# Kernel optimization log

Measured on AMD Instinct MI355X. Metric: run time of the kernel, lower is better.

## Reference

```python
import jax, jax.numpy as jnp
import numpy as np

H, K, D = 24, 2, 128          # query heads, kv heads, head_size
HIDDEN = H * D                # 3072
ROPE_THETA = 10000.0


def setup_inputs() -> dict:
    key = jax.random.key(0)
    ks = jax.random.split(key, 6)
    B, S = 2, 2048
    T = B * S
    hidden_states = jax.random.normal(ks[0], (T, HIDDEN), dtype=jnp.float32)
    w_qkv = jax.random.normal(ks[1], ((H + 2 * K) * D, HIDDEN), dtype=jnp.float32) * (HIDDEN ** -0.5)
    b_qkv = jax.random.normal(ks[2], ((H + 2 * K) * D,), dtype=jnp.float32) * 0.02
    w_o = jax.random.normal(ks[3], (HIDDEN, H * D), dtype=jnp.float32) * (HIDDEN ** -0.5)
    b_o = jax.random.normal(ks[4], (HIDDEN,), dtype=jnp.float32) * 0.02
    # rotary tables: positions restart per sequence (flash-varlen prefill layout)
    pos = jnp.tile(jnp.arange(S, dtype=jnp.float32), B)            # [T]
    inv_freq = 1.0 / (ROPE_THETA ** (jnp.arange(0, D, 2, dtype=jnp.float32) / D))  # [D/2]
    freqs = pos[:, None] * inv_freq[None, :]                        # [T, D/2]
    return {
        "hidden_states": hidden_states,
        "w_qkv": w_qkv, "b_qkv": b_qkv,
        "w_o": w_o, "b_o": b_o,
        "cos": jnp.cos(freqs), "sin": jnp.sin(freqs),
        "seq_len": S, "window": 1024,
    }


def _rope(x, cos, sin):
    # rotate-half (neox) style, as in TGI PositionRotaryEmbedding
    half = x.shape[-1] // 2
    x1, x2 = x[..., :half], x[..., half:]
    c, s = cos[:, None, :], sin[:, None, :]   # broadcast over head dim
    return jnp.concatenate([x1 * c - x2 * s, x2 * c + x1 * s], axis=-1)


def reference(hidden_states, w_qkv, b_qkv, w_o, b_o, cos, sin, seq_len, window):
    T = hidden_states.shape[0]
    B = T // seq_len
    scale = D ** -0.5

    # fused QKV projection
    qkv = hidden_states @ w_qkv.T + b_qkv                 # [T, (H+2K)*D]
    q = qkv[:, : H * D].reshape(T, H, D)
    kv = qkv[:, H * D:].reshape(T, 2, K, D)
    k, v = kv[:, 0], kv[:, 1]                             # [T, K, D]

    q = _rope(q, cos, sin)
    k = _rope(k, cos, sin)

    # GQA: expand kv heads to query heads
    groups = H // K
    qb = q.reshape(B, seq_len, H, D)
    kb = jnp.repeat(k.reshape(B, seq_len, K, D), groups, axis=2)  # [B,S,H,D]
    vb = jnp.repeat(v.reshape(B, seq_len, K, D), groups, axis=2)

    scores = jnp.einsum("bqhd,bkhd->bhqk", qb, kb) * scale        # [B,H,S,S]
    idx = jnp.arange(seq_len)
    delta = idx[:, None] - idx[None, :]
    mask = (delta >= 0) & (delta < window)                        # causal + sliding window
    scores = jnp.where(mask[None, None], scores, jnp.float32(-1e9))
    attn = jax.nn.softmax(scores, axis=-1)
    out = jnp.einsum("bhqk,bkhd->bqhd", attn, vb).reshape(T, H * D)
    return out @ w_o.T + b_o
```

## Files before the change

### kernel.cpp

```cpp
#include <hip/hip_runtime.h>
#include <hip/hip_bf16.h>

typedef __attribute__((ext_vector_type(8))) short bf16x8;
typedef __attribute__((ext_vector_type(4))) float f32x4;

__device__ __forceinline__ short f2bf_bits(float f) {
    __hip_bfloat16 h = __float2bfloat16(f);
    short s;
    __builtin_memcpy(&s, &h, 2);
    return s;
}

__device__ __forceinline__ float bf_bits2f(short s) {
    unsigned int u = ((unsigned int)(unsigned short)s) << 16;
    float f;
    __builtin_memcpy(&f, &u, 4);
    return f;
}

__device__ __forceinline__ bf16x8 load8(const float* p) {
    float4 a = *(const float4*)p;
    float4 b = *(const float4*)(p + 4);
    bf16x8 r;
    r[0] = f2bf_bits(a.x); r[1] = f2bf_bits(a.y);
    r[2] = f2bf_bits(a.z); r[3] = f2bf_bits(a.w);
    r[4] = f2bf_bits(b.x); r[5] = f2bf_bits(b.y);
    r[6] = f2bf_bits(b.z); r[7] = f2bf_bits(b.w);
    return r;
}
__device__ __forceinline__ bf16x8 load8(const __hip_bfloat16* p) {
    return *(const bf16x8*)p;
}

__device__ __forceinline__ void store_out(__hip_bfloat16* p, float v) {
    *p = __float2bfloat16(v);
}
__device__ __forceinline__ void store_out(float* p, float v) { *p = v; }

__global__ void cvt3_f32_bf16(const float* __restrict__ a, short* __restrict__ da, int na8,
                              const float* __restrict__ b, short* __restrict__ db, int nb8,
                              const float* __restrict__ c, short* __restrict__ dc, int nc8) {
    int i = blockIdx.x * 256 + threadIdx.x;
    if (i < na8) {
        *(bf16x8*)(da + (size_t)i * 8) = load8(a + (size_t)i * 8);
    } else if ((i -= na8) < nb8) {
        *(bf16x8*)(db + (size_t)i * 8) = load8(b + (size_t)i * 8);
    } else if ((i -= nb8) < nc8) {
        *(bf16x8*)(dc + (size_t)i * 8) = load8(c + (size_t)i * 8);
    }
}

#define GB_REG 65536

__device__ __forceinline__ int half_off(int buf, int half) {
    return buf * 32768 + half * 16384;
}

template <typename TC>
__global__ __launch_bounds__(512) void gemm256(
    const __hip_bfloat16* __restrict__ A, const __hip_bfloat16* __restrict__ B,
    const float* __restrict__ bias, TC* __restrict__ C, int M, int N, int K)
{
    __shared__ char smem[131072];

    const int tid  = threadIdx.x;
    const int lane = tid & 63;
    const int wid  = tid >> 6;
    const int quad = lane >> 4;
    const int m16  = lane & 15;
    const int wmg  = wid >> 2;
    const int wng  = wid & 3;
    const int bhalf = wng >> 1;
    const int bsub  = (wng & 1) * 4;

    const int gx  = gridDim.x;
    const int nwg = gx * gridDim.y;
    int lin = blockIdx.y * gx + blockIdx.x;
    if ((nwg & 7) == 0) {
        int q = nwg >> 3;
        lin = (lin & 7) * q + (lin >> 3);
    }
    const int bn = lin % gx, bm = lin / gx;
    const int mBase = bm * 256, nBase = bn * 256;

    const int roff = (m16 << 6) | ((quad * 16) ^ ((m16 & 8) << 2));

    int r_s[2], c_s[2];
    #pragma unroll
    for (int l = 0; l < 2; ++l) {
        int sub = l * 8 + wid;
        int r16 = (tid >> 2) & 15;
        int cb  = ((tid & 3) * 16) ^ ((r16 & 8) << 2);
        r_s[l] = (sub >> 1) * 16 + r16;
        c_s[l] = (sub & 1) * 32 + (cb >> 1);
    }

    const __hip_bfloat16* Ab = A + (size_t)mBase * K;
    const __hip_bfloat16* Bb = B + (size_t)nBase * K;

    auto stage = [&](int region, const __hip_bfloat16* base, int buf, int half, int tile) {
        const __hip_bfloat16* gb = base + (size_t)(half * 128) * K + tile * 64;
        #pragma unroll
        for (int l = 0; l < 2; ++l) {
            const __hip_bfloat16* g = gb + (size_t)r_s[l] * K + c_s[l];
            short* lb = (short*)(smem + region + half_off(buf, half) + l * 8192 + wid * 1024);
            __builtin_amdgcn_global_load_lds(
                (__attribute__((address_space(1))) void*)g,
                (__attribute__((address_space(3))) void*)lb, 16, 0, 0);
        }
    };

    f32x4 acc[8][4] = {};
    bf16x8 afr[4][2];
    bf16x8 bfr[2][2][2];

    auto LD_A = [&](int buf, int g) {
        const char* base = smem + half_off(buf, wmg) + (g ? 8192 : 0);
        #pragma unroll
        for (int m = 0; m < 4; ++m)
            #pragma unroll
            for (int ks = 0; ks < 2; ++ks)
                afr[m][ks] = *(const bf16x8*)(base + ((m * 2 + ks) << 10) + roff);
    };
    auto LD_B = [&](int buf, int g) {
        const char* base = smem + GB_REG + half_off(buf, bhalf) + ((bsub + g * 2) << 11);
        #pragma unroll
        for (int j = 0; j < 2; ++j)
            #pragma unroll
            for (int ks = 0; ks < 2; ++ks)
                bfr[g][j][ks] = *(const bf16x8*)(base + ((j * 2 + ks) << 10) + roff);
    };
    auto MM = [&](int mo, int g) {
        #pragma unroll
        for (int m = 0; m < 4; ++m)
            #pragma unroll
            for (int j = 0; j < 2; ++j)
                #pragma unroll
                for (int ks = 0; ks < 2; ++ks)
                    acc[mo + m][g * 2 + j] = __builtin_amdgcn_mfma_f32_16x16x32_bf16(
                        afr[m][ks], bfr[g][j][ks], acc[mo + m][g * 2 + j], 0, 0, 0);
    };

#define SBAR() __builtin_amdgcn_s_barrier()
#define WAIT_LGKM0() do { asm volatile("s_waitcnt lgkmcnt(0)" ::: "memory"); \
                          __builtin_amdgcn_sched_barrier(0); } while (0)
#define WAIT_VM4()   do { asm volatile("s_waitcnt vmcnt(4)"   ::: "memory"); \
                          __builtin_amdgcn_sched_barrier(0); } while (0)

    const int NT = K >> 6;

    stage(GB_REG, Bb, 0, 0, 0);
    stage(0,      Ab, 0, 0, 0);
    stage(GB_REG, Bb, 0, 1, 0);
    stage(0,      Ab, 0, 1, 0);
    stage(GB_REG, Bb, 1, 0, 1);
    stage(0,      Ab, 1, 0, 1);
    WAIT_VM4();
    SBAR();

    for (int i = 0; i < (NT >> 1); ++i) {
        const int to = 2 * i + 1;
        const int t2 = min(2 * i + 2, NT - 1);
        const int t3 = min(2 * i + 3, NT - 1);
        LD_A(0, 0); LD_B(0, 0);
        stage(GB_REG, Bb, 1, 1, to);
        SBAR(); WAIT_LGKM0();
        __builtin_amdgcn_s_setprio(1); MM(0, 0); __builtin_amdgcn_s_setprio(0);
        SBAR();
        LD_B(0, 1);
        stage(0, Ab, 1, 1, to);
        SBAR(); WAIT_LGKM0();
        __builtin_amdgcn_s_setprio(1); MM(0, 1); __builtin_amdgcn_s_setprio(0);
        SBAR();
        LD_A(0, 1);
        stage(GB_REG, Bb, 0, 0, t2);
        SBAR(); WAIT_LGKM0();
        __builtin_amdgcn_s_setprio(1); MM(4, 1); __builtin_amdgcn_s_setprio(0);
        SBAR();
        stage(0, Ab, 0, 0, t2);
        WAIT_VM4();
        SBAR();
        __builtin_amdgcn_s_setprio(1); MM(4, 0); __builtin_amdgcn_s_setprio(0);
        SBAR();
        LD_A(1, 0); LD_B(1, 0);
        stage(GB_REG, Bb, 0, 1, t2);
        SBAR(); WAIT_LGKM0();
        __builtin_amdgcn_s_setprio(1); MM(0, 0); __builtin_amdgcn_s_setprio(0);
        SBAR();
        LD_B(1, 1);
        stage(0, Ab, 0, 1, t2);
        SBAR(); WAIT_LGKM0();
        __builtin_amdgcn_s_setprio(1); MM(0, 1); __builtin_amdgcn_s_setprio(0);
        SBAR();
        LD_A(1, 1);
        stage(GB_REG, Bb, 1, 0, t3);
        SBAR(); WAIT_LGKM0();
        __builtin_amdgcn_s_setprio(1); MM(4, 1); __builtin_amdgcn_s_setprio(0);
        SBAR();
        stage(0, Ab, 1, 0, t3);
        WAIT_VM4();
        SBAR();
        __builtin_amdgcn_s_setprio(1); MM(4, 0); __builtin_amdgcn_s_setprio(0);
        SBAR();
    }

#undef SBAR
#undef WAIT_LGKM0
#undef WAIT_VM4

    float bv[4];
    #pragma unroll
    for (int j = 0; j < 4; ++j)
        bv[j] = bias[nBase + wng * 64 + j * 16 + m16];

    #pragma unroll
    for (int mf = 0; mf < 8; ++mf) {
        #pragma unroll
        for (int j = 0; j < 4; ++j) {
            const int col = nBase + wng * 64 + j * 16 + m16;
            #pragma unroll
            for (int r = 0; r < 4; ++r) {
                const int row = mBase + wmg * 128 + mf * 16 + quad * 4 + r;
                store_out(&C[(size_t)row * N + col], acc[mf][j][r] + bv[j]);
            }
        }
    }
}

#define LDSS 40

template <typename TA, typename TB, typename TC>
__global__ __launch_bounds__(256) void gemm_bt_bias(
    const TA* __restrict__ A, const TB* __restrict__ B,
    const float* __restrict__ bias, TC* __restrict__ C, int M, int N, int K)
{
    __shared__ short As[128 * LDSS];
    __shared__ short Bs[128 * LDSS];

    const int tid  = threadIdx.x;
    const int lane = tid & 63;
    const int wid  = tid >> 6;
    const int quad = lane >> 4;
    const int m16  = lane & 15;

    const int mBase = blockIdx.y * 128;
    const int nBase = blockIdx.x * 128;
    const int wm = (wid >> 1) * 64;
    const int wn = (wid & 1) * 64;

    f32x4 acc[4][4] = {};
    const int srow = tid >> 2;
    const int sgrp = (tid & 3) * 8;

    for (int kt = 0; kt < K; kt += 32) {
        __syncthreads();
        for (int p = 0; p < 2; ++p) {
            int r = srow + p * 64;
            *(bf16x8*)(&As[r * LDSS + sgrp]) =
                load8(A + (size_t)(mBase + r) * K + kt + sgrp);
            *(bf16x8*)(&Bs[r * LDSS + sgrp]) =
                load8(B + (size_t)(nBase + r) * K + kt + sgrp);
        }
        __syncthreads();

        bf16x8 afr[4], bfr[4];
        #pragma unroll
        for (int i = 0; i < 4; ++i)
            afr[i] = *(const bf16x8*)(&As[(wm + 16 * i + m16) * LDSS + quad * 8]);
        #pragma unroll
        for (int j = 0; j < 4; ++j)
            bfr[j] = *(const bf16x8*)(&Bs[(wn + 16 * j + m16) * LDSS + quad * 8]);
        #pragma unroll
        for (int i = 0; i < 4; ++i)
            #pragma unroll
            for (int j = 0; j < 4; ++j)
                acc[i][j] = __builtin_amdgcn_mfma_f32_16x16x32_bf16(
                    afr[i], bfr[j], acc[i][j], 0, 0, 0);
    }

    float bv[4];
    #pragma unroll
    for (int j = 0; j < 4; ++j)
        bv[j] = bias[nBase + wn + 16 * j + m16];

    #pragma unroll
    for (int i = 0; i < 4; ++i)
        #pragma unroll
        for (int j = 0; j < 4; ++j) {
            int col = nBase + wn + 16 * j + m16;
            #pragma unroll
            for (int r = 0; r < 4; ++r) {
                int row = mBase + wm + 16 * i + quad * 4 + r;
                store_out(&C[(size_t)row * N + col], acc[i][j][r] + bv[j]);
            }
        }
}

__global__ void rope_kernel(__hip_bfloat16* __restrict__ qkv,
                            const float* __restrict__ cosb,
                            const float* __restrict__ sinb, int T)
{
    int idx = blockIdx.x * 256 + threadIdx.x;
    int total = T * 26 * 8;
    if (idx >= total) return;
    int j = idx & 7;
    int h = (idx >> 3) % 26;
    int t = idx / (26 * 8);
    int col = (h < 24) ? h * 128 : 3072 + (h - 24) * 128;
    int d0 = j * 8;
    size_t base = (size_t)t * 3584 + col + d0;
    bf16x8 x1 = *(const bf16x8*)((const short*)qkv + base);
    bf16x8 x2 = *(const bf16x8*)((const short*)qkv + base + 64);
    float4 c0 = *(const float4*)(cosb + t * 64 + d0);
    float4 c1 = *(const float4*)(cosb + t * 64 + d0 + 4);
    float4 s0 = *(const float4*)(sinb + t * 64 + d0);
    float4 s1 = *(const float4*)(sinb + t * 64 + d0 + 4);
    float cc[8] = {c0.x, c0.y, c0.z, c0.w, c1.x, c1.y, c1.z, c1.w};
    float ss[8] = {s0.x, s0.y, s0.z, s0.w, s1.x, s1.y, s1.z, s1.w};
    bf16x8 o1, o2;
    #pragma unroll
    for (int i = 0; i < 8; ++i) {
        float f1 = bf_bits2f(x1[i]);
        float f2 = bf_bits2f(x2[i]);
        o1[i] = f2bf_bits(f1 * cc[i] - f2 * ss[i]);
        o2[i] = f2bf_bits(f2 * cc[i] + f1 * ss[i]);
    }
    *(bf16x8*)((short*)qkv + base)      = o1;
    *(bf16x8*)((short*)qkv + base + 64) = o2;
}

#define SM_SHIFT 12.0f

__global__ __launch_bounds__(256, 3) void attn_kernel(
    const __hip_bfloat16* __restrict__ qkv,
    __hip_bfloat16* __restrict__ out,
    const int* __restrict__ seq_len_p, const int* __restrict__ window_p)
{
    const int S = seq_len_p[0];
    const int window = window_p[0];
    const float scale = 0.088388347648318447f;

    const int h   = blockIdx.y;
    const int kvh = h / 12;
    const int tid  = threadIdx.x;
    const int lane = tid & 63;
    const int wid  = tid >> 6;
    const int quad = lane >> 4;
    const int m16  = lane & 15;

    const int qb_global = blockIdx.x * 128;
    const int b  = qb_global / S;
    const int qb = qb_global - b * S;

    __shared__ short Vt[128 * 72];
    __shared__ short Ps[4][32 * 40];

    const size_t kvrow0 = (size_t)(b * S) * 3584 + 3072 + kvh * 128;

    bf16x8 qf[2][4];
    {
        const __hip_bfloat16* qp =
            qkv + (size_t)(qb_global + wid * 32 + m16) * 3584 + h * 128;
        #pragma unroll
        for (int qt = 0; qt < 2; ++qt)
            #pragma unroll
            for (int dc = 0; dc < 4; ++dc)
                qf[qt][dc] = *(const bf16x8*)(qp + qt * 16 * 3584 + dc * 32 + quad * 8);
    }

    f32x4 accO[2][8] = {};
    float lqt[2] = {0.f, 0.f};

    int ka0 = qb - window + 1;
    if (ka0 < 0) ka0 = 0;
    ka0 &= ~31;
    const int kend = qb + 128;

    for (int kt = ka0; kt < kend; kt += 32) {
        __syncthreads();
        #pragma unroll
        for (int p = 0; p < 2; ++p) {
            int L   = tid + p * 256;
            int key = L & 31;
            int gg  = L >> 5;
            int d0  = gg * 8;
            bf16x8 v8 = *(const bf16x8*)(qkv + kvrow0 + (size_t)(kt + key) * 3584 + 256 + d0);
            short* dst = &Vt[d0 * 72 + key + (gg & 1) * 32];
            #pragma unroll
            for (int i2 = 0; i2 < 8; ++i2) dst[i2 * 72] = v8[i2];
        }
        __syncthreads();

        f32x4 sacc[2][2] = {};
        #pragma unroll
        for (int st = 0; st < 2; ++st) {
            const __hip_bfloat16* kp =
                qkv + kvrow0 + (size_t)(kt + st * 16 + m16) * 3584;
            #pragma unroll
            for (int dc = 0; dc < 4; ++dc) {
                bf16x8 kf = *(const bf16x8*)(kp + dc * 32 + quad * 8);
                sacc[st][0] = __builtin_amdgcn_mfma_f32_16x16x32_bf16(
                    kf, qf[0][dc], sacc[st][0], 0, 0, 0);
                sacc[st][1] = __builtin_amdgcn_mfma_f32_16x16x32_bf16(
                    kf, qf[1][dc], sacc[st][1], 0, 0, 0);
            }
        }

        #pragma unroll
        for (int qt = 0; qt < 2; ++qt) {
            const int qmin = qb + wid * 32 + qt * 16;
            short* prow = &Ps[wid][(qt * 16 + m16) * 40];
            float psum = 0.f;
            if (kt <= qmin - 31 && kt >= qmin + 16 - window) {
                #pragma unroll
                for (int st = 0; st < 2; ++st)
                    #pragma unroll
                    for (int r = 0; r < 4; ++r) {
                        float pp = __expf(fminf(
                            sacc[st][qt][r] * scale - SM_SHIFT, 80.f));
                        psum += pp;
                        prow[st * 16 + quad * 4 + r] = f2bf_bits(pp);
                    }
            } else {
                const int dl_base = (qmin + m16) - (kt + quad * 4);
                #pragma unroll
                for (int st = 0; st < 2; ++st)
                    #pragma unroll
                    for (int r = 0; r < 4; ++r) {
                        int dl = dl_base - st * 16 - r;
                        float pp = ((unsigned)dl < (unsigned)window)
                            ? __expf(fminf(sacc[st][qt][r] * scale - SM_SHIFT, 80.f))
                            : 0.f;
                        psum += pp;
                        prow[st * 16 + quad * 4 + r] = f2bf_bits(pp);
                    }
            }
            psum += __shfl_xor(psum, 16, 64);
            psum += __shfl_xor(psum, 32, 64);
            lqt[qt] += psum;
        }

        bf16x8 pf0 = *(const bf16x8*)(&Ps[wid][(0  + m16) * 40 + quad * 8]);
        bf16x8 pf1 = *(const bf16x8*)(&Ps[wid][(16 + m16) * 40 + quad * 8]);
        #pragma unroll
        for (int dt = 0; dt < 8; ++dt) {
            int row = dt * 16 + m16;
            bf16x8 vf = *(const bf16x8*)(&Vt[row * 72 + quad * 8 + ((row >> 3) & 1) * 32]);
            accO[0][dt] = __builtin_amdgcn_mfma_f32_16x16x32_bf16(pf0, vf, accO[0][dt], 0, 0, 0);
            accO[1][dt] = __builtin_amdgcn_mfma_f32_16x16x32_bf16(pf1, vf, accO[1][dt], 0, 0, 0);
        }
    }

    #pragma unroll
    for (int qt = 0; qt < 2; ++qt) {
        float li[4];
        #pragma unroll
        for (int r = 0; r < 4; ++r)
            li[r] = 1.0f / __shfl(lqt[qt], quad * 4 + r, 64);
        #pragma unroll
        for (int r = 0; r < 4; ++r) {
            int t = qb_global + wid * 32 + qt * 16 + quad * 4 + r;
            __hip_bfloat16* op = out + (size_t)t * 3072 + h * 128 + m16;
            #pragma unroll
            for (int dt = 0; dt < 8; ++dt)
                op[dt * 16] = __float2bfloat16(accO[qt][dt][r] * li[r]);
        }
    }
}

extern "C" void kernel_launch(void* const* d_in, const int* in_sizes, int n_in,
                              void* d_out, int out_size, void* d_ws, size_t ws_size,
                              hipStream_t stream) {
    const float* hidden = (const float*)d_in[0];
    const float* w_qkv  = (const float*)d_in[1];
    const float* b_qkv  = (const float*)d_in[2];
    const float* w_o    = (const float*)d_in[3];
    const float* b_o    = (const float*)d_in[4];
    const float* cosb   = (const float*)d_in[5];
    const float* sinb   = (const float*)d_in[6];
    const int* seq_len_p = (const int*)d_in[7];
    const int* window_p  = (const int*)d_in[8];

    const int HID  = in_sizes[4];
    const int NQKV = in_sizes[2];
    const int T    = in_sizes[0] / HID;

    size_t off = 0;
    auto alloc = [&](size_t bytes) {
        char* p = (char*)d_ws + off;
        off = (off + bytes + 255) & ~(size_t)255;
        return p;
    };
    __hip_bfloat16* qkv      = (__hip_bfloat16*)alloc((size_t)T * NQKV * 2);
    __hip_bfloat16* attn_out = (__hip_bfloat16*)alloc((size_t)T * HID * 2);
    __hip_bfloat16* hid_bf = (__hip_bfloat16*)alloc((size_t)T * HID * 2);
    __hip_bfloat16* wq_bf  = (__hip_bfloat16*)alloc((size_t)NQKV * HID * 2);
    __hip_bfloat16* wo_bf  = (__hip_bfloat16*)alloc((size_t)HID * HID * 2);
    const bool pre = (ws_size >= off);
    const bool big = pre && (T % 256 == 0) && (NQKV % 256 == 0) &&
                     (HID % 256 == 0) && (HID % 64 == 0);

    dim3 blk(256);

    if (big) {
        int n8h = T * HID / 8, n8q = NQKV * HID / 8, n8o = HID * HID / 8;
        int n8 = n8h + n8q + n8o;
        cvt3_f32_bf16<<<dim3((n8 + 255) / 256), blk, 0, stream>>>(
            hidden, (short*)hid_bf, n8h, w_qkv, (short*)wq_bf, n8q,
            w_o, (short*)wo_bf, n8o);
        gemm256<__hip_bfloat16><<<dim3(NQKV / 256, T / 256), dim3(512), 0, stream>>>(
            hid_bf, wq_bf, b_qkv, qkv, T, NQKV, HID);
    } else {
        gemm_bt_bias<float, float, __hip_bfloat16>
            <<<dim3(NQKV / 128, T / 128), blk, 0, stream>>>(
            hidden, w_qkv, b_qkv, qkv, T, NQKV, HID);
    }

    int total = T * 26 * 8;
    rope_kernel<<<dim3((total + 255) / 256), blk, 0, stream>>>(qkv, cosb, sinb, T);

    attn_kernel<<<dim3(T / 128, 24), blk, 0, stream>>>(qkv, attn_out, seq_len_p, window_p);

    if (big) {
        gemm256<float><<<dim3(HID / 256, T / 256), dim3(512), 0, stream>>>(
            attn_out, wo_bf, b_o, (float*)d_out, T, HID, HID);
    } else {
        gemm_bt_bias<__hip_bfloat16, float, float>
            <<<dim3(HID / 128, T / 128), blk, 0, stream>>>(
            attn_out, w_o, b_o, (float*)d_out, T, HID, HID);
    }
}
```

Before: 479.5 us.

## Double-buffer V tiles and prefetch K into registers in attention loop

The attention kernel now prefetches the next K tile into registers and the next V tile into a second LDS buffer while computing on the current one, leaving a single barrier per iteration. Query blocks are launched in reverse order so the blocks with the longest key ranges start first, and MFMA sections are wrapped in s_setprio. The intent is to hide global-load latency behind the MFMA work. In exchange, register and LDS use rise, so launch bounds drop from 3 to 2 blocks per CU, which lowers occupancy.

After: 484.1 us. No clear change (+1.0%).

```diff
diff --git a/kernel.cpp b/kernel.cpp
--- a/kernel.cpp
+++ b/kernel.cpp
@@ -331,7 +331,7 @@
 
 #define SM_SHIFT 12.0f
 
-__global__ __launch_bounds__(256, 3) void attn_kernel(
+__global__ __launch_bounds__(256, 2) void attn_kernel(
     const __hip_bfloat16* __restrict__ qkv,
     __hip_bfloat16* __restrict__ out,
     const int* __restrict__ seq_len_p, const int* __restrict__ window_p)
@@ -348,11 +348,13 @@
     const int quad = lane >> 4;
     const int m16  = lane & 15;
 
-    const int qb_global = blockIdx.x * 128;
-    const int b  = qb_global / S;
-    const int qb = qb_global - b * S;
-
-    __shared__ short Vt[128 * 72];
+    const int nbb = S >> 7;
+    const int b   = blockIdx.x / nbb;
+    const int ib  = blockIdx.x - b * nbb;
+    const int qb  = (nbb - 1 - ib) << 7;
+    const int qb_global = b * S + qb;
+
+    __shared__ short Vt[2][128 * 72];
     __shared__ short Ps[4][32 * 40];
 
     const size_t kvrow0 = (size_t)(b * S) * 3584 + 3072 + kvh * 128;
@@ -375,35 +377,67 @@
     if (ka0 < 0) ka0 = 0;
     ka0 &= ~31;
     const int kend = qb + 128;
-
-    for (int kt = ka0; kt < kend; kt += 32) {
-        __syncthreads();
-        #pragma unroll
-        for (int p = 0; p < 2; ++p) {
-            int L   = tid + p * 256;
-            int key = L & 31;
-            int gg  = L >> 5;
-            int d0  = gg * 8;
-            bf16x8 v8 = *(const bf16x8*)(qkv + kvrow0 + (size_t)(kt + key) * 3584 + 256 + d0);
-            short* dst = &Vt[d0 * 72 + key + (gg & 1) * 32];
-            #pragma unroll
-            for (int i2 = 0; i2 < 8; ++i2) dst[i2 * 72] = v8[i2];
-        }
-        __syncthreads();
+    const int niter = (kend - ka0) >> 5;
+
+    const int skey = tid & 31;
+    const int sgg0 = tid >> 5;
+    const int sgg1 = sgg0 + 8;
+
+    bf16x8 vnx0, vnx1;
+    vnx0 = *(const bf16x8*)(qkv + kvrow0 + (size_t)(ka0 + skey) * 3584 + 256 + sgg0 * 8);
+    vnx1 = *(const bf16x8*)(qkv + kvrow0 + (size_t)(ka0 + skey) * 3584 + 256 + sgg1 * 8);
+    bf16x8 kreg[2][4];
+    {
+        const __hip_bfloat16* kp = qkv + kvrow0 + (size_t)ka0 * 3584;
+        #pragma unroll
+        for (int st = 0; st < 2; ++st)
+            #pragma unroll
+            for (int dc = 0; dc < 4; ++dc)
+                kreg[st][dc] = *(const bf16x8*)(kp + (size_t)(st * 16 + m16) * 3584 + dc * 32 + quad * 8);
+    }
+    {
+        short* dst0 = &Vt[0][(sgg0 * 8) * 72 + skey + (sgg0 & 1) * 32];
+        short* dst1 = &Vt[0][(sgg1 * 8) * 72 + skey + (sgg1 & 1) * 32];
+        #pragma unroll
+        for (int i2 = 0; i2 < 8; ++i2) dst0[i2 * 72] = vnx0[i2];
+        #pragma unroll
+        for (int i2 = 0; i2 < 8; ++i2) dst1[i2 * 72] = vnx1[i2];
+    }
+    asm volatile("s_waitcnt lgkmcnt(0)" ::: "memory");
+    __builtin_amdgcn_s_barrier();
+    __builtin_amdgcn_sched_barrier(0);
+
+    for (int it = 0; it < niter; ++it) {
+        const int kt  = ka0 + it * 32;
+        const int buf = it & 1;
+        const bool notlast = (it + 1 < niter);
+        const int ktn = notlast ? kt + 32 : kt;
+
+        if (notlast) {
+            vnx0 = *(const bf16x8*)(qkv + kvrow0 + (size_t)(ktn + skey) * 3584 + 256 + sgg0 * 8);
+            vnx1 = *(const bf16x8*)(qkv + kvrow0 + (size_t)(ktn + skey) * 3584 + 256 + sgg1 * 8);
+        }
 
         f32x4 sacc[2][2] = {};
-        #pragma unroll
-        for (int st = 0; st < 2; ++st) {
-            const __hip_bfloat16* kp =
-                qkv + kvrow0 + (size_t)(kt + st * 16 + m16) * 3584;
+        __builtin_amdgcn_s_setprio(1);
+        #pragma unroll
+        for (int st = 0; st < 2; ++st)
             #pragma unroll
             for (int dc = 0; dc < 4; ++dc) {
-                bf16x8 kf = *(const bf16x8*)(kp + dc * 32 + quad * 8);
                 sacc[st][0] = __builtin_amdgcn_mfma_f32_16x16x32_bf16(
-                    kf, qf[0][dc], sacc[st][0], 0, 0, 0);
+                    kreg[st][dc], qf[0][dc], sacc[st][0], 0, 0, 0);
                 sacc[st][1] = __builtin_amdgcn_mfma_f32_16x16x32_bf16(
-                    kf, qf[1][dc], sacc[st][1], 0, 0, 0);
+                    kreg[st][dc], qf[1][dc], sacc[st][1], 0, 0, 0);
             }
+        __builtin_amdgcn_s_setprio(0);
+
+        if (notlast) {
+            const __hip_bfloat16* kp = qkv + kvrow0 + (size_t)ktn * 3584;
+            #pragma unroll
+            for (int st = 0; st < 2; ++st)
+                #pragma unroll
+                for (int dc = 0; dc < 4; ++dc)
+                    kreg[st][dc] = *(const bf16x8*)(kp + (size_t)(st * 16 + m16) * 3584 + dc * 32 + quad * 8);
         }
 
         #pragma unroll
@@ -440,15 +474,32 @@
             lqt[qt] += psum;
         }
 
-        bf16x8 pf0 = *(const bf16x8*)(&Ps[wid][(0  + m16) * 40 + quad * 8]);
-        bf16x8 pf1 = *(const bf16x8*)(&Ps[wid][(16 + m16) * 40 + quad * 8]);
-        #pragma unroll
-        for (int dt = 0; dt < 8; ++dt) {
-            int row = dt * 16 + m16;
-            bf16x8 vf = *(const bf16x8*)(&Vt[row * 72 + quad * 8 + ((row >> 3) & 1) * 32]);
-            accO[0][dt] = __builtin_amdgcn_mfma_f32_16x16x32_bf16(pf0, vf, accO[0][dt], 0, 0, 0);
-            accO[1][dt] = __builtin_amdgcn_mfma_f32_16x16x32_bf16(pf1, vf, accO[1][dt], 0, 0, 0);
-        }
+        {
+            bf16x8 pf0 = *(const bf16x8*)(&Ps[wid][(0  + m16) * 40 + quad * 8]);
+            bf16x8 pf1 = *(const bf16x8*)(&Ps[wid][(16 + m16) * 40 + quad * 8]);
+            __builtin_amdgcn_s_setprio(1);
+            #pragma unroll
+            for (int dt = 0; dt < 8; ++dt) {
+                int row = dt * 16 + m16;
+                bf16x8 vf = *(const bf16x8*)(&Vt[buf][row * 72 + quad * 8 + ((row >> 3) & 1) * 32]);
+                accO[0][dt] = __builtin_amdgcn_mfma_f32_16x16x32_bf16(pf0, vf, accO[0][dt], 0, 0, 0);
+                accO[1][dt] = __builtin_amdgcn_mfma_f32_16x16x32_bf16(pf1, vf, accO[1][dt], 0, 0, 0);
+            }
+            __builtin_amdgcn_s_setprio(0);
+        }
+
+        if (notlast) {
+            short* dst0 = &Vt[buf ^ 1][(sgg0 * 8) * 72 + skey + (sgg0 & 1) * 32];
+            short* dst1 = &Vt[buf ^ 1][(sgg1 * 8) * 72 + skey + (sgg1 & 1) * 32];
+            #pragma unroll
+            for (int i2 = 0; i2 < 8; ++i2) dst0[i2 * 72] = vnx0[i2];
+            #pragma unroll
+            for (int i2 = 0; i2 < 8; ++i2) dst1[i2 * 72] = vnx1[i2];
+        }
+
+        asm volatile("s_waitcnt lgkmcnt(0)" ::: "memory");
+        __builtin_amdgcn_s_barrier();
+        __builtin_amdgcn_sched_barrier(0);
     }
 
     #pragma unroll
```

## Halve attention query tile to 64, reverse block order, prefetch V before barrier

Applied to the files above, without the earlier changes.

The attention kernel now processes 64 query rows per block (16 per wave) instead of 128, doubling the grid and raising the occupancy target to 4 blocks per CU. Blocks are issued in reverse order within each sequence, so the longer causal tiles start first. V loads are issued before the barrier using raw s_barrier with an explicit waitcnt, and the PV MFMAs are wrapped in setprio to favour the matrix work. Smaller tiles give more parallelism and less register pressure, but each K/V tile is reused by fewer queries, which raises K/V load traffic per output row.

Result: slower. 644.0 us (+34.3%).

```diff
diff --git a/kernel.cpp b/kernel.cpp
--- a/kernel.cpp
+++ b/kernel.cpp
@@ -331,7 +331,7 @@
 
 #define SM_SHIFT 12.0f
 
-__global__ __launch_bounds__(256, 3) void attn_kernel(
+__global__ __launch_bounds__(256, 4) void attn_kernel(
     const __hip_bfloat16* __restrict__ qkv,
     __hip_bfloat16* __restrict__ out,
     const int* __restrict__ seq_len_p, const int* __restrict__ window_p)
@@ -348,50 +348,60 @@
     const int quad = lane >> 4;
     const int m16  = lane & 15;
 
-    const int qb_global = blockIdx.x * 128;
-    const int b  = qb_global / S;
-    const int qb = qb_global - b * S;
+    const int nbb = S >> 6;
+    const int b   = blockIdx.x / nbb;
+    const int ib  = blockIdx.x - b * nbb;
+    const int qb  = (nbb - 1 - ib) << 6;
+    const int qb_global = b * S + qb;
 
     __shared__ short Vt[128 * 72];
-    __shared__ short Ps[4][32 * 40];
+    __shared__ short Ps[4][16 * 40];
 
     const size_t kvrow0 = (size_t)(b * S) * 3584 + 3072 + kvh * 128;
 
-    bf16x8 qf[2][4];
+    bf16x8 qf[4];
     {
         const __hip_bfloat16* qp =
-            qkv + (size_t)(qb_global + wid * 32 + m16) * 3584 + h * 128;
-        #pragma unroll
-        for (int qt = 0; qt < 2; ++qt)
-            #pragma unroll
-            for (int dc = 0; dc < 4; ++dc)
-                qf[qt][dc] = *(const bf16x8*)(qp + qt * 16 * 3584 + dc * 32 + quad * 8);
-    }
-
-    f32x4 accO[2][8] = {};
-    float lqt[2] = {0.f, 0.f};
+            qkv + (size_t)(qb_global + wid * 16 + m16) * 3584 + h * 128;
+        #pragma unroll
+        for (int dc = 0; dc < 4; ++dc)
+            qf[dc] = *(const bf16x8*)(qp + dc * 32 + quad * 8);
+    }
+
+    f32x4 accO[8] = {};
+    float lq = 0.f;
 
     int ka0 = qb - window + 1;
     if (ka0 < 0) ka0 = 0;
     ka0 &= ~31;
-    const int kend = qb + 128;
-
-    for (int kt = ka0; kt < kend; kt += 32) {
-        __syncthreads();
-        #pragma unroll
-        for (int p = 0; p < 2; ++p) {
-            int L   = tid + p * 256;
-            int key = L & 31;
-            int gg  = L >> 5;
-            int d0  = gg * 8;
-            bf16x8 v8 = *(const bf16x8*)(qkv + kvrow0 + (size_t)(kt + key) * 3584 + 256 + d0);
-            short* dst = &Vt[d0 * 72 + key + (gg & 1) * 32];
-            #pragma unroll
-            for (int i2 = 0; i2 < 8; ++i2) dst[i2 * 72] = v8[i2];
-        }
-        __syncthreads();
-
-        f32x4 sacc[2][2] = {};
+    const int kend = qb + 64;
+    const int niter = (kend - ka0) >> 5;
+
+    const int skey = tid & 31;
+    const int sgg0 = tid >> 5;
+    const int sgg1 = sgg0 + 8;
+
+    for (int it = 0; it < niter; ++it) {
+        const int kt = ka0 + it * 32;
+
+        bf16x8 v0 = *(const bf16x8*)(qkv + kvrow0 + (size_t)(kt + skey) * 3584 + 256 + sgg0 * 8);
+        bf16x8 v1 = *(const bf16x8*)(qkv + kvrow0 + (size_t)(kt + skey) * 3584 + 256 + sgg1 * 8);
+
+        __builtin_amdgcn_s_barrier();
+
+        {
+            short* dst0 = &Vt[(sgg0 * 8) * 72 + skey + (sgg0 & 1) * 32];
+            short* dst1 = &Vt[(sgg1 * 8) * 72 + skey + (sgg1 & 1) * 32];
+            #pragma unroll
+            for (int i2 = 0; i2 < 8; ++i2) dst0[i2 * 72] = v0[i2];
+            #pragma unroll
+            for (int i2 = 0; i2 < 8; ++i2) dst1[i2 * 72] = v1[i2];
+        }
+        asm volatile("s_waitcnt lgkmcnt(0)" ::: "memory");
+        __builtin_amdgcn_s_barrier();
+        __builtin_amdgcn_sched_barrier(0);
+
+        f32x4 sacc[2] = {};
         #pragma unroll
         for (int st = 0; st < 2; ++st) {
             const __hip_bfloat16* kp =
@@ -399,17 +409,14 @@
             #pragma unroll
             for (int dc = 0; dc < 4; ++dc) {
                 bf16x8 kf = *(const bf16x8*)(kp + dc * 32 + quad * 8);
-                sacc[st][0] = __builtin_amdgcn_mfma_f32_16x16x32_bf16(
-                    kf, qf[0][dc], sacc[st][0], 0, 0, 0);
-                sacc[st][1] = __builtin_amdgcn_mfma_f32_16x16x32_bf16(
-                    kf, qf[1][dc], sacc[st][1], 0, 0, 0);
+                sacc[st] = __builtin_amdgcn_mfma_f32_16x16x32_bf16(
+                    kf, qf[dc], sacc[st], 0, 0, 0);
             }
         }
 
-        #pragma unroll
-        for (int qt = 0; qt < 2; ++qt) {
-            const int qmin = qb + wid * 32 + qt * 16;
-            short* prow = &Ps[wid][(qt * 16 + m16) * 40];
+        {
+            const int qmin = qb + wid * 16;
+            short* prow = &Ps[wid][m16 * 40];
             float psum = 0.f;
             if (kt <= qmin - 31 && kt >= qmin + 16 - window) {
                 #pragma unroll
@@ -417,7 +424,7 @@
                     #pragma unroll
                     for (int r = 0; r < 4; ++r) {
                         float pp = __expf(fminf(
-                            sacc[st][qt][r] * scale - SM_SHIFT, 80.f));
+                            sacc[st][r] * scale - SM_SHIFT, 80.f));
                         psum += pp;
                         prow[st * 16 + quad * 4 + r] = f2bf_bits(pp);
                     }
@@ -429,7 +436,7 @@
                     for (int r = 0; r < 4; ++r) {
                         int dl = dl_base - st * 16 - r;
                         float pp = ((unsigned)dl < (unsigned)window)
-                            ? __expf(fminf(sacc[st][qt][r] * scale - SM_SHIFT, 80.f))
+                            ? __expf(fminf(sacc[st][r] * scale - SM_SHIFT, 80.f))
                             : 0.f;
                         psum += pp;
                         prow[st * 16 + quad * 4 + r] = f2bf_bits(pp);
@@ -437,33 +444,34 @@
             }
             psum += __shfl_xor(psum, 16, 64);
             psum += __shfl_xor(psum, 32, 64);
-            lqt[qt] += psum;
-        }
-
-        bf16x8 pf0 = *(const bf16x8*)(&Ps[wid][(0  + m16) * 40 + quad * 8]);
-        bf16x8 pf1 = *(const bf16x8*)(&Ps[wid][(16 + m16) * 40 + quad * 8]);
-        #pragma unroll
-        for (int dt = 0; dt < 8; ++dt) {
-            int row = dt * 16 + m16;
-            bf16x8 vf = *(const bf16x8*)(&Vt[row * 72 + quad * 8 + ((row >> 3) & 1) * 32]);
-            accO[0][dt] = __builtin_amdgcn_mfma_f32_16x16x32_bf16(pf0, vf, accO[0][dt], 0, 0, 0);
-            accO[1][dt] = __builtin_amdgcn_mfma_f32_16x16x32_bf16(pf1, vf, accO[1][dt], 0, 0, 0);
-        }
-    }
-
-    #pragma unroll
-    for (int qt = 0; qt < 2; ++qt) {
+            lq += psum;
+        }
+
+        {
+            bf16x8 pf = *(const bf16x8*)(&Ps[wid][m16 * 40 + quad * 8]);
+            __builtin_amdgcn_s_setprio(1);
+            #pragma unroll
+            for (int dt = 0; dt < 8; ++dt) {
+                int row = dt * 16 + m16;
+                bf16x8 vf = *(const bf16x8*)(&Vt[row * 72 + quad * 8 + ((row >> 3) & 1) * 32]);
+                accO[dt] = __builtin_amdgcn_mfma_f32_16x16x32_bf16(pf, vf, accO[dt], 0, 0, 0);
+            }
+            __builtin_amdgcn_s_setprio(0);
+        }
+    }
+
+    {
         float li[4];
         #pragma unroll
         for (int r = 0; r < 4; ++r)
-            li[r] = 1.0f / __shfl(lqt[qt], quad * 4 + r, 64);
+            li[r] = 1.0f / __shfl(lq, quad * 4 + r, 64);
         #pragma unroll
         for (int r = 0; r < 4; ++r) {
-            int t = qb_global + wid * 32 + qt * 16 + quad * 4 + r;
+            int t = qb_global + wid * 16 + quad * 4 + r;
             __hip_bfloat16* op = out + (size_t)t * 3072 + h * 128 + m16;
             #pragma unroll
             for (int dt = 0; dt < 8; ++dt)
-                op[dt * 16] = __float2bfloat16(accO[qt][dt][r] * li[r]);
+                op[dt * 16] = __float2bfloat16(accO[dt][r] * li[r]);
         }
     }
 }
@@ -519,7 +527,7 @@
     int total = T * 26 * 8;
     rope_kernel<<<dim3((total + 255) / 256), blk, 0, stream>>>(qkv, cosb, sinb, T);
 
-    attn_kernel<<<dim3(T / 128, 24), blk, 0, stream>>>(qkv, attn_out, seq_len_p, window_p);
+    attn_kernel<<<dim3(T / 64, 24), blk, 0, stream>>>(qkv, attn_out, seq_len_p, window_p);
 
     if (big) {
         gemm256<float><<<dim3(HID / 256, T / 256), dim3(512), 0, stream>>>(
```
